# Optimization experiments

Measured on AMD Instinct MI355X. Metric: run time of the kernel, lower is better.

The kernel has to match this reference:

```python
import jax, jax.numpy as jnp
import numpy as np

N = 2048          # nodes
IN_DIM = 512      # in_dim
H = 8             # num_heads
HD = IN_DIM // H  # head_dim = 64
L = 5             # max_path_len
E = 32768         # edges
D_EDGE = 64       # edge_feat_dim


def setup_inputs() -> dict:
    key = jax.random.key(0)
    ks = jax.random.split(key, 14)
    w = 1.0 / np.sqrt(IN_DIM)
    return {
        "node_feat": jax.random.normal(ks[0], (N, IN_DIM), jnp.float32),
        "edge_index": jax.random.randint(ks[1], (2, E), 0, N, dtype=jnp.int32),
        "max_path_len": 5,
        "shortest_distances": jax.random.randint(ks[2], (N, N), 0, L + 1, dtype=jnp.int32),
        "shortest_paths": jax.random.randint(ks[3], (N, N, L), 0, E + 1, dtype=jnp.int32),  # E == padding row
        "edge_feat": jax.random.normal(ks[4], (E, D_EDGE), jnp.float32),
        "attention_mask": jnp.zeros((N, N), jnp.int32),
        "WQ": jax.random.normal(ks[5], (IN_DIM, IN_DIM), jnp.float32) * w,
        "bQ": jax.random.normal(ks[6], (IN_DIM,), jnp.float32) * 0.02,
        "WK": jax.random.normal(ks[7], (IN_DIM, IN_DIM), jnp.float32) * w,
        "bK": jax.random.normal(ks[8], (IN_DIM,), jnp.float32) * 0.02,
        "WV": jax.random.normal(ks[9], (IN_DIM, IN_DIM), jnp.float32) * w,
        "bV": jax.random.normal(ks[10], (IN_DIM,), jnp.float32) * 0.02,
        "WO": jax.random.normal(ks[11], (IN_DIM, IN_DIM), jnp.float32) * w,
        "bO": jnp.zeros((IN_DIM,), jnp.float32),
        "spatial_bias": jax.random.normal(ks[12], ((L + 1) * H, 1), jnp.float32) * 0.02,
        "edge_weight": jax.random.normal(ks[13], ((L + 1) * H, D_EDGE), jnp.float32) * 0.02,
    }


def reference(node_feat, edge_index, max_path_len, shortest_distances, shortest_paths,
              edge_feat, attention_mask, WQ, bQ, WK, bK, WV, bV, WO, bO,
              spatial_bias, edge_weight):
    Nn, D = node_feat.shape
    Lp = max_path_len  # min(max_path_len, max_shortest_path_len); distances reach Lp here

    Q = (node_feat @ WQ + bQ).reshape(Nn, H, HD)
    K = (node_feat @ WK + bK).reshape(Nn, H, HD)
    V = (node_feat @ WV + bV).reshape(Nn, H, HD)

    # QK^T / sqrt(head_dim), laid out [N, N, H] as in the original after permute
    scores = jnp.einsum('nhd,mhd->nmh', Q, K) / np.sqrt(HD).astype(np.float32)

    # SpatialEncoding: bias table [(L+1)*H, 1] -> [L+1, H]; gather by clamped distance
    sp_table = spatial_bias.reshape(Lp + 1, H)
    dist = jnp.clip(shortest_distances, 0, Lp)
    scores = scores + sp_table[dist]  # [N, N, H]

    # EdgeEncoding: einsum('xyld,ldh->xyh') refactored as per-edge projection then gather
    W_e = edge_weight[: Lp * H].reshape(Lp, H, D_EDGE)  # (reshape[L,H,D].permute -> [L,D,H])
    padded = jnp.concatenate([edge_feat, jnp.zeros((1, D_EDGE), edge_feat.dtype)], axis=0)
    T = jnp.einsum('ed,lhd->elh', padded, W_e)  # [E+1, L, H]
    sp = shortest_paths[:, :, :Lp]
    gathered = T[sp, jnp.arange(Lp)[None, None, :]]  # [N, N, L, H]
    scores = scores + gathered.sum(axis=2)

    mask = attention_mask.astype(bool)
    scores = jnp.where(mask[:, :, None], -jnp.inf, scores)

    # NOTE: original applies softmax over dim=-1 of the [N, N, H] tensor (the head axis);
    # faithfully reproduced here. Dropout is identity (eval / p for inference).
    attn = jax.nn.softmax(scores, axis=-1)

    out = jnp.einsum('nmh,mhd->nhd', attn, V).reshape(Nn, D)
    return out @ WO + bO
```

## Files before the change

### kernel.cpp

```cpp
#include <hip/hip_runtime.h>

#define NN     2048
#define DIM    512
#define NH     8
#define HD     64
#define NE     32768
#define EPAD   32832
#define CHUNKS 8
#define CHSZ   (NN/CHUNKS)
#define NJT    (CHSZ/64)
#define LOG2E  1.4426950408889634f

typedef __attribute__((ext_vector_type(8))) short bf16x8;
typedef __attribute__((ext_vector_type(4))) float f32x4;

#define MFMA(a,b,c) __builtin_amdgcn_mfma_f32_16x16x32_bf16((a),(b),(c),0,0,0)

__device__ __forceinline__ float bf2f(unsigned int u16){
  union { unsigned int i; float f; } v; v.i = u16 << 16; return v.f;
}
__device__ __forceinline__ unsigned short f2bf(float f){
  union { float ff; unsigned int i; } v; v.ff = f;
  return (unsigned short)((v.i + 0x7fffu + ((v.i >> 16) & 1u)) >> 16);
}

__global__ __launch_bounds__(256) void cvt_k(
    const float* __restrict__ X, const float* __restrict__ ef, const float* __restrict__ ew,
    unsigned short* __restrict__ Xb, unsigned short* __restrict__ pEF, unsigned short* __restrict__ pEW)
{
  long g = (long)blockIdx.x*256 + threadIdx.x;
  const long GX = (long)NN*DIM/8;
  const long GE = (long)EPAD*8;
  const float* src; unsigned short* dst; long off, lim8;
  if (g < GX){ src = X;  dst = Xb;  off = g;        lim8 = GX; }
  else if (g < GX+GE){ src = ef; dst = pEF; off = g-GX; lim8 = (long)NE*8; }
  else { off = g-GX-GE; if (off >= 512) return; src = ew; dst = pEW; lim8 = 320; }
  unsigned short o[8];
  if (off < lim8){
    #pragma unroll
    for (int i=0;i<8;i++) o[i] = f2bf(src[off*8+i]);
  } else {
    #pragma unroll
    for (int i=0;i<8;i++) o[i] = 0;
  }
  *(uint4*)(dst + off*8) = *(const uint4*)o;
}

__global__ __launch_bounds__(256) void transpose512(
    const float* __restrict__ a0, const float* __restrict__ a1,
    const float* __restrict__ a2, const float* __restrict__ a3,
    unsigned short* __restrict__ out)
{
  __shared__ unsigned short tile[32][33];
  const float* src = blockIdx.z==0 ? a0 : blockIdx.z==1 ? a1 : blockIdx.z==2 ? a2 : a3;
  unsigned short* dst = out + (size_t)blockIdx.z*DIM*DIM;
  int bx = blockIdx.x*32, by = blockIdx.y*32;
  int tx = threadIdx.x, ty = threadIdx.y;
  #pragma unroll
  for (int i=0;i<32;i+=8) tile[ty+i][tx] = f2bf(src[(size_t)(by+ty+i)*DIM + bx+tx]);
  __syncthreads();
  #pragma unroll
  for (int i=0;i<32;i+=8) dst[(size_t)(bx+ty+i)*DIM + by+tx] = tile[tx][ty+i];
}

__global__ __launch_bounds__(256) void gemm_bt(
    const unsigned short* __restrict__ A1, const unsigned short* __restrict__ A2,
    const float* __restrict__ bias, unsigned short* __restrict__ C, float* __restrict__ Cf,
    int M, int N, int K, int bias_row)
{
  int lane = threadIdx.x & 63, w = threadIdx.x >> 6;
  int quad = lane >> 4, low = lane & 15;
  int m0 = blockIdx.y*64 + w*16;
  int n0 = blockIdx.x*32;
  f32x4 acc[2];
  acc[0] = (f32x4){0.f,0.f,0.f,0.f};
  acc[1] = (f32x4){0.f,0.f,0.f,0.f};
  for (int k0=0; k0<K; k0+=32){
    bf16x8 a = *(const bf16x8*)(A1 + (size_t)(m0+low)*K + k0 + quad*8);
    #pragma unroll
    for (int t=0;t<2;t++){
      bf16x8 b = *(const bf16x8*)(A2 + (size_t)(n0+16*t+low)*K + k0 + quad*8);
      acc[t] = MFMA(a, b, acc[t]);
    }
  }
  #pragma unroll
  for (int t=0;t<2;t++){
    #pragma unroll
    for (int r=0;r<4;r++){
      int row = m0 + quad*4 + r;
      int col = n0 + 16*t + low;
      float v = acc[t][r];
      if (bias) v += bias[bias_row ? row : col];
      if (Cf) Cf[(size_t)row*N + col] = v;
      else    C [(size_t)row*N + col] = f2bf(v);
    }
  }
}

__global__ __launch_bounds__(512) void attn_k(
    const unsigned short* __restrict__ Qb, const unsigned short* __restrict__ Kb,
    const unsigned short* __restrict__ Vt, const unsigned short* __restrict__ T2,
    const float* __restrict__ spb, const int* __restrict__ dist,
    const int* __restrict__ sp, const int* __restrict__ maskp,
    float* __restrict__ partO)
{
  __shared__ __attribute__((aligned(16))) float sld[NH][16][68];
  __shared__ float sptab[48];
  int tid = threadIdx.x;
  int lane = tid & 63, h = tid >> 6;
  int quad = lane >> 4, low = lane & 15;
  int q0 = blockIdx.x * 16;
  int chunk = blockIdx.y;
  if (tid < 48) sptab[tid] = spb[tid];

  bf16x8 aq[2];
  #pragma unroll
  for (int s=0;s<2;s++)
    aq[s] = *(const bf16x8*)(Qb + (size_t)(q0+low)*DIM + h*HD + s*32 + quad*8);

  f32x4 accO[4];
  #pragma unroll
  for (int t=0;t<4;t++) accO[t] = (f32x4){0.f,0.f,0.f,0.f};

  int pd[2], pm[2], pe[2][5];
  #pragma unroll
  for (int it=0; it<2; ++it){
    int p = tid + it*512;
    int qq = p >> 6, mm = p & 63;
    long pix = (long)(q0+qq)*NN + (chunk*CHSZ + mm);
    pd[it] = dist[pix]; pm[it] = maskp[pix];
    #pragma unroll
    for (int l=0;l<5;l++) pe[it][l] = sp[pix*5 + l];
  }
  __syncthreads();

  for (int jt=0; jt<NJT; ++jt){
    int m0 = chunk*CHSZ + jt*64;

    float bb[2][8];
    int mk[2];
    #pragma unroll
    for (int it=0; it<2; ++it){
      mk[it] = pm[it];
      int dd = pd[it];
      dd = dd < 0 ? 0 : (dd > 5 ? 5 : dd);
      #pragma unroll
      for (int x=0;x<8;x++) bb[it][x] = sptab[dd*8 + x];
      #pragma unroll
      for (int l=0;l<5;l++){
        int e = pe[it][l];
        if ((unsigned)e > (unsigned)NE) e = NE;
        uint4 tv = *(const uint4*)(T2 + (size_t)e*64 + l*8);
        bb[it][0] += bf2f(tv.x & 0xffffu); bb[it][1] += bf2f(tv.x >> 16);
        bb[it][2] += bf2f(tv.y & 0xffffu); bb[it][3] += bf2f(tv.y >> 16);
        bb[it][4] += bf2f(tv.z & 0xffffu); bb[it][5] += bf2f(tv.z >> 16);
        bb[it][6] += bf2f(tv.w & 0xffffu); bb[it][7] += bf2f(tv.w >> 16);
      }
    }

    __syncthreads();

    #pragma unroll
    for (int it=0; it<2; ++it){
      int p = tid + it*512;
      int qq = p >> 6, mm = p & 63;
      #pragma unroll
      for (int x=0;x<8;x++) sld[x][qq][mm] = mk[it] ? -1e30f : bb[it][x];
    }

    if (jt+1 < NJT){
      #pragma unroll
      for (int it=0; it<2; ++it){
        int p = tid + it*512;
        int qq = p >> 6, mm = p & 63;
        long pix = (long)(q0+qq)*NN + (m0 + 64 + mm);
        pd[it] = dist[pix]; pm[it] = maskp[pix];
        #pragma unroll
        for (int l=0;l<5;l++) pe[it][l] = sp[pix*5 + l];
      }
    }
    __syncthreads();

    f32x4 S[4];
    #pragma unroll
    for (int t=0;t<4;t++) S[t] = (f32x4){0.f,0.f,0.f,0.f};
    #pragma unroll
    for (int s=0;s<2;s++){
      #pragma unroll
      for (int t=0;t<4;t++){
        bf16x8 bk = *(const bf16x8*)(Kb + (size_t)(m0+16*t+low)*DIM + h*HD + s*32 + quad*8);
        S[t] = MFMA(aq[s], bk, S[t]);
      }
    }
    #pragma unroll
    for (int t=0;t<4;t++){
      #pragma unroll
      for (int r=0;r<4;r++){
        float* slot = &sld[h][quad*4+r][low+16*t];
        *slot = S[t][r]*0.125f + *slot;
      }
    }
    __syncthreads();

    #pragma unroll
    for (int it=0; it<2; ++it){
      int p = tid + it*512;
      int qq = p >> 6, mm = p & 63;
      float s0[8];
      #pragma unroll
      for (int x=0;x<8;x++) s0[x] = sld[x][qq][mm];
      float mx = s0[0];
      #pragma unroll
      for (int x=1;x<8;x++) mx = fmaxf(mx, s0[x]);
      float sum = 0.f;
      #pragma unroll
      for (int x=0;x<8;x++){ s0[x] = exp2f((s0[x]-mx)*LOG2E); sum += s0[x]; }
      float inv = (mx < -1e29f) ? 0.f : 1.f/sum;
      #pragma unroll
      for (int x=0;x<8;x++) sld[x][qq][mm] = s0[x]*inv;
    }
    __syncthreads();

    bf16x8 ap[2];
    #pragma unroll
    for (int s=0;s<2;s++){
      const float* pp = &sld[h][low][s*32 + quad*8];
      float4 x0 = *(const float4*)pp;
      float4 x1 = *(const float4*)(pp + 4);
      bf16x8 a;
      a[0]=(short)f2bf(x0.x); a[1]=(short)f2bf(x0.y); a[2]=(short)f2bf(x0.z); a[3]=(short)f2bf(x0.w);
      a[4]=(short)f2bf(x1.x); a[5]=(short)f2bf(x1.y); a[6]=(short)f2bf(x1.z); a[7]=(short)f2bf(x1.w);
      ap[s] = a;
    }
    #pragma unroll
    for (int s=0;s<2;s++){
      #pragma unroll
      for (int t=0;t<4;t++){
        bf16x8 bv = *(const bf16x8*)(Vt + (size_t)(h*HD + 16*t + low)*NN + m0 + s*32 + quad*8);
        accO[t] = MFMA(ap[s], bv, accO[t]);
      }
    }
  }

  #pragma unroll
  for (int t=0;t<4;t++){
    #pragma unroll
    for (int r=0;r<4;r++){
      int q = quad*4 + r;
      partO[(((size_t)chunk*NN + q0 + q)*NH + h)*HD + 16*t + low] = accO[t][r];
    }
  }
}

__global__ __launch_bounds__(512) void merge_k(const float* __restrict__ partO,
                                               unsigned short* __restrict__ Obf)
{
  size_t idx = (size_t)blockIdx.x*512 + threadIdx.x;
  float s = 0.f;
  #pragma unroll
  for (int c=0;c<CHUNKS;c++) s += partO[(size_t)c*NN*DIM + idx];
  Obf[idx] = f2bf(s);
}

extern "C" void kernel_launch(void* const* d_in, const int* in_sizes, int n_in,
                              void* d_out, int out_size, void* d_ws, size_t ws_size,
                              hipStream_t stream)
{
  const float* X    = (const float*)d_in[0];
  const int*  dist  = (const int*)d_in[3];
  const int*  sp    = (const int*)d_in[4];
  const float* ef   = (const float*)d_in[5];
  const int*  maskp = (const int*)d_in[6];
  const float* WQ   = (const float*)d_in[7];
  const float* bQ   = (const float*)d_in[8];
  const float* WK   = (const float*)d_in[9];
  const float* bK   = (const float*)d_in[10];
  const float* WV   = (const float*)d_in[11];
  const float* bV   = (const float*)d_in[12];
  const float* WO   = (const float*)d_in[13];
  const float* bO   = (const float*)d_in[14];
  const float* spb  = (const float*)d_in[15];
  const float* ew   = (const float*)d_in[16];

  char* ws = (char*)d_ws;
  unsigned short* Wt   = (unsigned short*)(ws + 0);
  unsigned short* Xb   = (unsigned short*)(ws + 2097152);
  unsigned short* Qb   = (unsigned short*)(ws + 4194304);
  unsigned short* Kb   = (unsigned short*)(ws + 6291456);
  unsigned short* Vtb  = (unsigned short*)(ws + 8388608);
  unsigned short* pEF  = (unsigned short*)(ws + 10485760);
  unsigned short* pEW  = (unsigned short*)(ws + 14688256);
  unsigned short* T2   = (unsigned short*)(ws + 14696448);
  unsigned short* Obf  = (unsigned short*)(ws + 18898944);
  float*          pO   = (float*)(ws + 20996096);

  cvt_k<<<dim3(1540), dim3(256), 0, stream>>>(X, ef, ew, Xb, pEF, pEW);
  transpose512<<<dim3(16,16,4), dim3(32,8), 0, stream>>>(WQ, WK, WV, WO, Wt);
  gemm_bt<<<dim3(2,513),  dim3(256), 0, stream>>>(pEF, pEW, (const float*)nullptr, T2, (float*)nullptr, EPAD, 64, 64, 0);
  gemm_bt<<<dim3(16,32),  dim3(256), 0, stream>>>(Xb,  Wt,          bQ, Qb,  (float*)nullptr, NN, DIM, DIM, 0);
  gemm_bt<<<dim3(16,32),  dim3(256), 0, stream>>>(Xb,  Wt + 262144, bK, Kb,  (float*)nullptr, NN, DIM, DIM, 0);
  gemm_bt<<<dim3(64,8),   dim3(256), 0, stream>>>(Wt + 524288, Xb,  bV, Vtb, (float*)nullptr, DIM, NN, DIM, 1);
  attn_k<<<dim3(128,CHUNKS), dim3(512), 0, stream>>>(Qb, Kb, Vtb, T2, spb, dist, sp, maskp, pO);
  merge_k<<<dim3(2048), dim3(512), 0, stream>>>(pO, Obf);
  gemm_bt<<<dim3(16,32), dim3(256), 0, stream>>>(Obf, Wt + 786432, bO, (unsigned short*)nullptr, (float*)d_out, NN, DIM, DIM, 0);
}
```

Before: 411.0 us.

## Precompute attention bias in a separate gather kernel and halve key chunks

The spatial-bias and edge-path gather plus the mask are moved out of the attention kernel into a new bias_k kernel. bias_k writes a packed bf16 per-pixel, per-head bias tensor of N*N*8 values. The attention kernel then streams one 16-byte vector per pixel instead of doing dependent random T2 gathers inside its main loop, which is meant to remove latency stalls there. The cost is an extra large intermediate write and read, plus bias rounding to bf16. The key-dimension split is also reduced from 8 to 4 chunks, which gives fewer partial outputs to merge but fewer attention blocks.

```diff
diff --git a/kernel.cpp b/kernel.cpp
--- a/kernel.cpp
+++ b/kernel.cpp
@@ -6,13 +6,14 @@
 #define HD     64
 #define NE     32768
 #define EPAD   32832
-#define CHUNKS 8
+#define CHUNKS 4
 #define CHSZ   (NN/CHUNKS)
 #define NJT    (CHSZ/64)
 #define LOG2E  1.4426950408889634f
 
 typedef __attribute__((ext_vector_type(8))) short bf16x8;
 typedef __attribute__((ext_vector_type(4))) float f32x4;
+typedef __attribute__((ext_vector_type(4))) unsigned int u32x4;
 
 #define MFMA(a,b,c) __builtin_amdgcn_mfma_f32_16x16x32_bf16((a),(b),(c),0,0,0)
 
@@ -97,21 +98,52 @@
   }
 }
 
+__global__ __launch_bounds__(256) void bias_k(
+    const unsigned short* __restrict__ T2, const float* __restrict__ spb,
+    const int* __restrict__ dist, const int* __restrict__ sp, const int* __restrict__ maskp,
+    unsigned short* __restrict__ biasB)
+{
+  __shared__ float sptab[48];
+  if (threadIdx.x < 48) sptab[threadIdx.x] = spb[threadIdx.x];
+  __syncthreads();
+  long pix = (long)blockIdx.x*256 + threadIdx.x;
+  int dd = __builtin_nontemporal_load(dist + pix);
+  int mk = __builtin_nontemporal_load(maskp + pix);
+  int e[5];
+  #pragma unroll
+  for (int l=0;l<5;l++) e[l] = __builtin_nontemporal_load(sp + pix*5 + l);
+  dd = dd < 0 ? 0 : (dd > 5 ? 5 : dd);
+  float b[8];
+  #pragma unroll
+  for (int x=0;x<8;x++) b[x] = sptab[dd*8 + x];
+  #pragma unroll
+  for (int l=0;l<5;l++){
+    int ee = e[l];
+    if ((unsigned)ee > (unsigned)NE) ee = NE;
+    uint4 tv = *(const uint4*)(T2 + (size_t)ee*64 + l*8);
+    b[0] += bf2f(tv.x & 0xffffu); b[1] += bf2f(tv.x >> 16);
+    b[2] += bf2f(tv.y & 0xffffu); b[3] += bf2f(tv.y >> 16);
+    b[4] += bf2f(tv.z & 0xffffu); b[5] += bf2f(tv.z >> 16);
+    b[6] += bf2f(tv.w & 0xffffu); b[7] += bf2f(tv.w >> 16);
+  }
+  unsigned short o[8];
+  #pragma unroll
+  for (int x=0;x<8;x++) o[x] = mk ? f2bf(-1e30f) : f2bf(b[x]);
+  u32x4 ov = *(const u32x4*)o;
+  __builtin_nontemporal_store(ov, (u32x4*)(biasB + pix*8));
+}
+
 __global__ __launch_bounds__(512) void attn_k(
     const unsigned short* __restrict__ Qb, const unsigned short* __restrict__ Kb,
-    const unsigned short* __restrict__ Vt, const unsigned short* __restrict__ T2,
-    const float* __restrict__ spb, const int* __restrict__ dist,
-    const int* __restrict__ sp, const int* __restrict__ maskp,
+    const unsigned short* __restrict__ Vt, const unsigned short* __restrict__ biasB,
     float* __restrict__ partO)
 {
   __shared__ __attribute__((aligned(16))) float sld[NH][16][68];
-  __shared__ float sptab[48];
   int tid = threadIdx.x;
   int lane = tid & 63, h = tid >> 6;
   int quad = lane >> 4, low = lane & 15;
   int q0 = blockIdx.x * 16;
   int chunk = blockIdx.y;
-  if (tid < 48) sptab[tid] = spb[tid];
 
   bf16x8 aq[2];
   #pragma unroll
@@ -122,61 +154,34 @@
   #pragma unroll
   for (int t=0;t<4;t++) accO[t] = (f32x4){0.f,0.f,0.f,0.f};
 
-  int pd[2], pm[2], pe[2][5];
+  uint4 pb[2];
   #pragma unroll
   for (int it=0; it<2; ++it){
     int p = tid + it*512;
     int qq = p >> 6, mm = p & 63;
-    long pix = (long)(q0+qq)*NN + (chunk*CHSZ + mm);
-    pd[it] = dist[pix]; pm[it] = maskp[pix];
-    #pragma unroll
-    for (int l=0;l<5;l++) pe[it][l] = sp[pix*5 + l];
-  }
-  __syncthreads();
+    pb[it] = *(const uint4*)(biasB + ((size_t)(q0+qq)*NN + chunk*CHSZ + mm)*8);
+  }
 
   for (int jt=0; jt<NJT; ++jt){
     int m0 = chunk*CHSZ + jt*64;
-
-    float bb[2][8];
-    int mk[2];
-    #pragma unroll
-    for (int it=0; it<2; ++it){
-      mk[it] = pm[it];
-      int dd = pd[it];
-      dd = dd < 0 ? 0 : (dd > 5 ? 5 : dd);
-      #pragma unroll
-      for (int x=0;x<8;x++) bb[it][x] = sptab[dd*8 + x];
-      #pragma unroll
-      for (int l=0;l<5;l++){
-        int e = pe[it][l];
-        if ((unsigned)e > (unsigned)NE) e = NE;
-        uint4 tv = *(const uint4*)(T2 + (size_t)e*64 + l*8);
-        bb[it][0] += bf2f(tv.x & 0xffffu); bb[it][1] += bf2f(tv.x >> 16);
-        bb[it][2] += bf2f(tv.y & 0xffffu); bb[it][3] += bf2f(tv.y >> 16);
-        bb[it][4] += bf2f(tv.z & 0xffffu); bb[it][5] += bf2f(tv.z >> 16);
-        bb[it][6] += bf2f(tv.w & 0xffffu); bb[it][7] += bf2f(tv.w >> 16);
-      }
-    }
-
     __syncthreads();
 
     #pragma unroll
     for (int it=0; it<2; ++it){
       int p = tid + it*512;
       int qq = p >> 6, mm = p & 63;
-      #pragma unroll
-      for (int x=0;x<8;x++) sld[x][qq][mm] = mk[it] ? -1e30f : bb[it][x];
-    }
-
+      uint4 tv = pb[it];
+      sld[0][qq][mm] = bf2f(tv.x & 0xffffu); sld[1][qq][mm] = bf2f(tv.x >> 16);
+      sld[2][qq][mm] = bf2f(tv.y & 0xffffu); sld[3][qq][mm] = bf2f(tv.y >> 16);
+      sld[4][qq][mm] = bf2f(tv.z & 0xffffu); sld[5][qq][mm] = bf2f(tv.z >> 16);
+      sld[6][qq][mm] = bf2f(tv.w & 0xffffu); sld[7][qq][mm] = bf2f(tv.w >> 16);
+    }
     if (jt+1 < NJT){
       #pragma unroll
       for (int it=0; it<2; ++it){
         int p = tid + it*512;
         int qq = p >> 6, mm = p & 63;
-        long pix = (long)(q0+qq)*NN + (m0 + 64 + mm);
-        pd[it] = dist[pix]; pm[it] = maskp[pix];
-        #pragma unroll
-        for (int l=0;l<5;l++) pe[it][l] = sp[pix*5 + l];
+        pb[it] = *(const uint4*)(biasB + ((size_t)(q0+qq)*NN + m0 + 64 + mm)*8);
       }
     }
     __syncthreads();
@@ -292,15 +297,17 @@
   unsigned short* pEW  = (unsigned short*)(ws + 14688256);
   unsigned short* T2   = (unsigned short*)(ws + 14696448);
   unsigned short* Obf  = (unsigned short*)(ws + 18898944);
-  float*          pO   = (float*)(ws + 20996096);
+  unsigned short* biasB= (unsigned short*)(ws + 20996096);
+  float*          pO   = (float*)(ws + 88104960);
 
   cvt_k<<<dim3(1540), dim3(256), 0, stream>>>(X, ef, ew, Xb, pEF, pEW);
   transpose512<<<dim3(16,16,4), dim3(32,8), 0, stream>>>(WQ, WK, WV, WO, Wt);
   gemm_bt<<<dim3(2,513),  dim3(256), 0, stream>>>(pEF, pEW, (const float*)nullptr, T2, (float*)nullptr, EPAD, 64, 64, 0);
+  bias_k<<<dim3(NN*NN/256), dim3(256), 0, stream>>>(T2, spb, dist, sp, maskp, biasB);
   gemm_bt<<<dim3(16,32),  dim3(256), 0, stream>>>(Xb,  Wt,          bQ, Qb,  (float*)nullptr, NN, DIM, DIM, 0);
   gemm_bt<<<dim3(16,32),  dim3(256), 0, stream>>>(Xb,  Wt + 262144, bK, Kb,  (float*)nullptr, NN, DIM, DIM, 0);
   gemm_bt<<<dim3(64,8),   dim3(256), 0, stream>>>(Wt + 524288, Xb,  bV, Vtb, (float*)nullptr, DIM, NN, DIM, 1);
-  attn_k<<<dim3(128,CHUNKS), dim3(512), 0, stream>>>(Qb, Kb, Vtb, T2, spb, dist, sp, maskp, pO);
+  attn_k<<<dim3(128,CHUNKS), dim3(512), 0, stream>>>(Qb, Kb, Vtb, biasB, pO);
   merge_k<<<dim3(2048), dim3(512), 0, stream>>>(pO, Obf);
   gemm_bt<<<dim3(16,32), dim3(256), 0, stream>>>(Obf, Wt + 786432, bO, (unsigned short*)nullptr, (float*)d_out, NN, DIM, DIM, 0);
 }
```

Measured after the change: 426.9 us. 1.04x slower.
